# Kernel optimization log

Hardware: AMD Instinct MI355X
Metric: run time of the kernel (lower is better)

Reference implementation:

```python
import jax, jax.numpy as jnp
import numpy as np

N = 65536      # voxels
NFIX = 4096    # fixed-BC voxels (x == 0)
H = 128        # MLP hidden width
NFORCE = 4096  # force-surface points
E0 = 1.0
NU = 0.3
PENAL = 3.0
EM_V = 1e-3    # element volume
L_FIX = 0.05   # BC ramp length for analytical fixed-BC scale
K_FIX = E0 * 100.0
NUM_HUTCH = 50


def mlp(params, x):
    W1, b1, W2, b2, W3, b3, W4, b4 = params
    h = jnp.tanh(x @ W1 + b1)
    h = jnp.tanh(h @ W2 + b2)
    h = jnp.tanh(h @ W3 + b3)
    return h @ W4 + b4


def bc_scale(coord):
    # analytical fixed-BC scale: 0 exactly on the fixed face (x==0), ramps to 1
    return jnp.clip(coord[..., 0] / L_FIX, 0.0, 1.0)


def hutchinson_trace(params, coords, key, num_samples=NUM_HUTCH):
    # tr(J J^T) estimate via v^T J J^T v = ||J^T v||^2, batched VJPs (replaces
    # the per-sample autograd.grad python loop).
    out, vjp_fn = jax.vjp(lambda p: mlp(p, coords), params)

    def step(acc, k):
        v = jax.random.normal(k, out.shape, dtype=out.dtype)
        (g,) = vjp_fn(v)
        flat = jnp.concatenate([x.reshape(-1) for x in jax.tree_util.tree_leaves(g)])
        return acc + flat @ flat, None

    keys = jax.random.split(key, num_samples)
    tot, _ = jax.lax.scan(step, jnp.float32(0.0), keys)
    return tot / num_samples


def setup_inputs() -> dict:
    key = jax.random.key(0)
    ks = jax.random.split(key, 12)
    coord = jax.random.uniform(ks[0], (N, 3), dtype=jnp.float32)
    coord = coord.at[:, 0].set(0.02 + 0.98 * coord[:, 0])  # free voxels: x > 0
    coord = coord.at[:NFIX, 0].set(0.0)                    # fixed voxels: x == 0
    xPhys_m = jax.random.uniform(ks[1], (N, 1), dtype=jnp.float32)
    def lin(k, fi, fo):
        return jax.random.normal(k, (fi, fo), dtype=jnp.float32) / jnp.sqrt(jnp.float32(fi))
    W1 = lin(ks[2], 3, H); b1 = jnp.zeros((H,), jnp.float32)
    W2 = lin(ks[3], H, H); b2 = jnp.zeros((H,), jnp.float32)
    W3 = lin(ks[4], H, H); b3 = jnp.zeros((H,), jnp.float32)
    W4 = lin(ks[5], H, 3); b4 = jnp.zeros((3,), jnp.float32)
    force_coords = jax.random.uniform(ks[6], (NFORCE, 3), dtype=jnp.float32)
    F_vector = jax.random.normal(ks[7], (3,), dtype=jnp.float32)
    return dict(xPhys_m=xPhys_m, coord=coord, W1=W1, b1=b1, W2=W2, b2=b2,
                W3=W3, b3=b3, W4=W4, b4=b4, force_coords=force_coords,
                F_vector=F_vector, n_fix=NFIX)


def reference(xPhys_m, coord, W1, b1, W2, b2, W3, b3, W4, b4,
              force_coords, F_vector, n_fix):
    params = (W1, b1, W2, b2, W3, b3, W4, b4)

    u = mlp(params, coord)                       # [N,3] displacements
    scale = bc_scale(coord)                      # [N]
    fixed_mask = (scale == 0.0)

    # fixed-BC penalty energy
    u_fix = u * fixed_mask[:, None].astype(u.dtype)
    E_fix_all = xPhys_m ** PENAL * 0.5 * K_FIX * jnp.sum(u_fix ** 2, axis=1, keepdims=True)
    n_fix_ratio = jnp.float32(n_fix) / jnp.float32(N)
    E_fix = jnp.mean(E_fix_all[:n_fix]) * n_fix_ratio * EM_V

    # NTK-based adaptive weight via Hutchinson trace (detached, like .item())
    hkey = jax.random.key(42)
    ku, kr = jax.random.split(hkey)
    tr_uu = hutchinson_trace(params, coord[:n_fix], ku)
    tr_rr = hutchinson_trace(params, coord[n_fix:], kr)
    lam_fix = jax.lax.stop_gradient(jnp.clip(tr_rr / (tr_uu + 1e-12), 1e-3, 1e3))

    # per-voxel displacement Jacobian J[n, i, j] = d u_i / d coord_j  (batched
    # fwd-mode replaces three autograd.grad calls)
    J = jax.vmap(jax.jacfwd(lambda c: mlp(params, c)))(coord)  # [N,3,3]
    ux = J[:, 1, :]   # grads of u[:,1] (u0 in source)
    uy = J[:, 0, :]   # grads of u[:,0] (u1 in source)
    uz = J[:, 2, :]
    eps11 = ux[:, 1]
    eps12 = 0.5 * ux[:, 0] + 0.5 * uy[:, 1]
    eps13 = 0.5 * ux[:, 2] + 0.5 * uz[:, 1]
    eps22 = uy[:, 0]
    eps23 = 0.5 * uy[:, 2] + 0.5 * uz[:, 0]
    eps33 = uz[:, 2]

    lame_mu = E0 / (2.0 * (1.0 + NU))
    lame_lambda = E0 * NU / ((1.0 + NU) * (1.0 - 2.0 * NU))
    tr_strain = eps11 + eps22 + eps33
    sq_diag = eps11 * eps11 + eps22 * eps22 + eps33 * eps33
    energy = (0.5 * lame_lambda * tr_strain * tr_strain
              + lame_mu * (sq_diag + 2.0 * (eps12 * eps12 + eps13 * eps13 + eps23 * eps23)))
    energy = energy[:, None] * xPhys_m ** PENAL   # [N,1]
    energy_c = energy * 2.0
    energy_ans = EM_V * jnp.mean(energy)

    force_l = jnp.sum(mlp(params, force_coords) @ F_vector)

    loss = energy_ans - force_l + lam_fix * E_fix
    return (loss, energy_c, u)
```

## Files before the change

kernel.cpp:

```cpp
#include <hip/hip_runtime.h>
#include <math.h>

typedef __bf16 bf16x8 __attribute__((ext_vector_type(8)));
typedef __bf16 bf16x4 __attribute__((ext_vector_type(4)));
typedef float f32x4 __attribute__((ext_vector_type(4)));

#define HDIM 128
#define NTHREADS 512

#define EMV 0.001f
#define LFIX 0.05f
#define KFIX 100.0f
#define LAMBDA_L 0.5769230769230769f
#define MU_L 0.3846153846153846f

__device__ __forceinline__ int swb(int r, int blk) {
    return (r << 7) + ((blk ^ (r & 7)) << 3);
}
__device__ __forceinline__ int swb32(int r, int g) {
    return (r << 5) + ((g ^ ((r >> 1) & 3)) << 3);
}

__device__ __forceinline__ float fast_tanh(float x) {
    float xc = fminf(fmaxf(x, -10.f), 10.f);
    float e = __expf(2.f * xc);
    return (e - 1.f) / (e + 1.f);
}

__device__ __forceinline__ float wred(float v) {
#pragma unroll
    for (int off = 32; off > 0; off >>= 1) v += __shfl_down(v, off, 64);
    return v;
}

template <int NB, int CT0, int CT1>
__device__ __forceinline__ void gemm_f8(const bf16x8 (&aw)[4],
                                        __bf16* const* inb, __bf16* const* outb,
                                        const float* __restrict__ bsL,
                                        int wid, int l15, int q) {
    f32x4 acc[NB][CT1 - CT0];
#pragma unroll
    for (int b = 0; b < NB; ++b)
#pragma unroll
        for (int c = 0; c < CT1 - CT0; ++c) acc[b][c] = (f32x4){0.f, 0.f, 0.f, 0.f};

#pragma unroll
    for (int s = 0; s < 4; ++s)
#pragma unroll
        for (int b = 0; b < NB; ++b)
#pragma unroll
            for (int c = CT0; c < CT1; ++c) {
                bf16x8 bfr = *(const bf16x8*)(inb[b] + swb(c * 16 + l15, s * 4 + q));
                acc[b][c - CT0] = __builtin_amdgcn_mfma_f32_16x16x32_bf16(
                    aw[s], bfr, acc[b][c - CT0], 0, 0, 0);
            }
    __syncthreads();
    const int n0 = wid * 16 + q * 4;
    float4 bv = *(const float4*)(bsL + n0);
    float bias4[4] = {bv.x, bv.y, bv.z, bv.w};
#pragma unroll
    for (int c = CT0; c < CT1; ++c) {
        const int p = c * 16 + l15;
        const int widx = swb(p, n0 >> 3) + (n0 & 7);
        bf16x4 hv;
        float fct[4];
#pragma unroll
        for (int i = 0; i < 4; ++i) {
            float h = fast_tanh(acc[0][c - CT0][i] + bias4[i]);
            hv[i] = (__bf16)h;
            fct[i] = 1.f - h * h;
        }
        *(bf16x4*)(outb[0] + widx) = hv;
#pragma unroll
        for (int b = 1; b < NB; ++b) {
            bf16x4 ov;
#pragma unroll
            for (int i = 0; i < 4; ++i) ov[i] = (__bf16)(acc[b][c - CT0][i] * fct[i]);
            *(bf16x4*)(outb[b] + widx) = ov;
        }
    }
}

template <int NB>
__device__ __forceinline__ void gemm_tr8(const float* __restrict__ Wg, __bf16* Wst,
                                         __bf16* const* bufs,
                                         const __bf16* __restrict__ href,
                                         int wid, int l15, int q, int tid) {
    f32x4 acc[NB][2];
#pragma unroll
    for (int b = 0; b < NB; ++b) {
        acc[b][0] = (f32x4){0.f, 0.f, 0.f, 0.f};
        acc[b][1] = (f32x4){0.f, 0.f, 0.f, 0.f};
    }
#pragma unroll
    for (int c = 0; c < 4; ++c) {
        __syncthreads();
        {
            int j = tid >> 2, k8 = tid & 3;
            const float4* src = (const float4*)(Wg + j * HDIM + c * 32 + k8 * 8);
            float4 v0 = src[0], v1 = src[1];
            bf16x8 pk = {(__bf16)v0.x, (__bf16)v0.y, (__bf16)v0.z, (__bf16)v0.w,
                         (__bf16)v1.x, (__bf16)v1.y, (__bf16)v1.z, (__bf16)v1.w};
            *(bf16x8*)(Wst + swb32(j, k8)) = pk;
        }
        __syncthreads();
        bf16x8 afr = *(const bf16x8*)(Wst + swb32(wid * 16 + l15, q));
#pragma unroll
        for (int b = 0; b < NB; ++b) {
            bf16x8 b0 = *(const bf16x8*)(bufs[b] + swb(l15, c * 4 + q));
            acc[b][0] = __builtin_amdgcn_mfma_f32_16x16x32_bf16(afr, b0, acc[b][0], 0, 0, 0);
            bf16x8 b1 = *(const bf16x8*)(bufs[b] + swb(16 + l15, c * 4 + q));
            acc[b][1] = __builtin_amdgcn_mfma_f32_16x16x32_bf16(afr, b1, acc[b][1], 0, 0, 0);
        }
    }
    __syncthreads();
    const int n0 = wid * 16 + q * 4;
#pragma unroll
    for (int ct = 0; ct < 2; ++ct) {
        const int p = ct * 16 + l15;
        const int widx = swb(p, n0 >> 3) + (n0 & 7);
        bf16x4 hv = *(const bf16x4*)(href + widx);
        float fct[4];
#pragma unroll
        for (int i = 0; i < 4; ++i) {
            float h = (float)hv[i];
            fct[i] = 1.f - h * h;
        }
#pragma unroll
        for (int b = 0; b < NB; ++b) {
            bf16x4 ov;
#pragma unroll
            for (int i = 0; i < 4; ++i) ov[i] = (__bf16)(acc[b][ct][i] * fct[i]);
            *(bf16x4*)(bufs[b] + widx) = ov;
        }
    }
}

__device__ __forceinline__ void dnorms8(const __bf16* a, const __bf16* b, const __bf16* c2,
                                        float* npart, int tid) {
    int p = tid & 31, cc = tid >> 5;
    bf16x8 v0 = *(const bf16x8*)(a + swb(p, cc));
    bf16x8 v1 = *(const bf16x8*)(b + swb(p, cc));
    bf16x8 v2 = *(const bf16x8*)(c2 + swb(p, cc));
    float s0 = 0.f, s1 = 0.f, s2 = 0.f;
#pragma unroll
    for (int e = 0; e < 8; ++e) {
        float f0 = (float)v0[e], f1 = (float)v1[e], f2 = (float)v2[e];
        s0 += f0 * f0;
        s1 += f1 * f1;
        s2 += f2 * f2;
    }
    npart[(0 + cc) * 32 + p] = s0;
    npart[(16 + cc) * 32 + p] = s1;
    npart[(32 + cc) * 32 + p] = s2;
}

__device__ __forceinline__ float sum16(const float* npart, int buf, int p) {
    float d = 0.f;
#pragma unroll
    for (int i = 0; i < 16; ++i) d += npart[(buf * 16 + i) * 32 + p];
    return d;
}
__device__ __forceinline__ float sum48(const float* npart, int p) {
    float d = 0.f;
#pragma unroll
    for (int i = 0; i < 48; ++i) d += npart[i * 32 + p];
    return d;
}

__global__ void __launch_bounds__(NTHREADS, 4) pinn_all(
    const float* __restrict__ xPhys, const float* __restrict__ coord,
    const float* __restrict__ W1, const float* __restrict__ b1,
    const float* __restrict__ W2, const float* __restrict__ b2,
    const float* __restrict__ W3, const float* __restrict__ b3,
    const float* __restrict__ W4, const float* __restrict__ b4,
    const float* __restrict__ fc, const float* __restrict__ Fv,
    const int* __restrict__ nfixp,
    float* __restrict__ energy_c_out, float* __restrict__ u_out,
    float* __restrict__ acc, int nm32, int nmain64, int ntrb, int NF) {
    __shared__ __align__(16) __bf16 pool[32768];
    __shared__ __align__(16) __bf16 W4p[16 * HDIM];
    __shared__ __align__(16) float W1s[4 * HDIM];
    __shared__ __align__(16) float W4ts[3 * HDIM];
    __shared__ __align__(16) float gls[64 * 12];
    __shared__ __align__(16) float uls[64 * 4];
    __shared__ float nh1s[32], nh2s[32], nh3s[32];

    const int tid = threadIdx.x;
    const int lane = tid & 63, wid = tid >> 6, l15 = lane & 15, q = lane >> 4;
    const int bi = blockIdx.x;
    const int nfixv = nfixp[0];

    int ttile = -1;
    if (bi < ntrb) {
        const int nfull = nfixv >> 5;
        const int cm = (nfixv & 31) ? 1 : 0;
        const int c1 = (nfull + 7) >> 3;
        int t;
        if (bi < c1) {
            t = bi << 3;
        } else if (cm && bi == c1) {
            t = nfull;
        } else {
            const int rr0 = nfull + cm;
            const int f0 = rr0 + ((8 - (rr0 & 15) + 16) & 15);
            t = f0 + ((bi - c1 - cm) << 4);
        }
        if (t >= nm32) return;
        ttile = t;
    }

    for (int i = tid; i < 3 * HDIM; i += NTHREADS) W1s[i] = W1[i];
    if (tid < HDIM) W1s[3 * HDIM + tid] = b1[tid];
    if (tid < 3 * HDIM) W4ts[tid] = W4[(tid & 127) * 3 + (tid >> 7)];
    if (tid < 256) {
        int o = tid >> 4, blk = tid & 15, j0 = blk * 8;
        bf16x8 pk;
#pragma unroll
        for (int e = 0; e < 8; ++e) pk[e] = (__bf16)((o < 3) ? W4[(j0 + e) * 3 + o] : 0.f);
        *(bf16x8*)(W4p + swb(o, blk)) = pk;
    }
    bf16x8 aw2[4], aw3[4];
#pragma unroll
    for (int s = 0; s < 4; ++s) {
        const int kb = s * 32 + q * 8;
        const int n = wid * 16 + l15;
        bf16x8 v2, v3;
#pragma unroll
        for (int e = 0; e < 8; ++e) {
            v2[e] = (__bf16)W2[(kb + e) * HDIM + n];
            v3[e] = (__bf16)W3[(kb + e) * HDIM + n];
        }
        aw2[s] = v2;
        aw3[s] = v3;
    }
    __syncthreads();

    if (bi < ntrb) {
        const int base = ttile * 32;
        __bf16* H1 = pool;
        __bf16* H2 = pool + 4096;
        __bf16* H3 = pool + 8192;
        __bf16* T0 = pool + 12288;
        __bf16* T1 = pool + 16384;
        __bf16* T2 = pool + 20480;
        __bf16* WST = pool + 24576;
        float* npart = (float*)(pool + 28672);

        {
            int p = tid >> 4, blk = tid & 15, j0 = blk * 8;
            const float* cp = coord + (base + p) * 3;
            float x0 = cp[0], x1 = cp[1], x2 = cp[2];
            bf16x8 hv, t0v, t1v, t2v;
#pragma unroll
            for (int jj = 0; jj < 8; ++jj) {
                int j = j0 + jj;
                float w0 = W1s[j], w1 = W1s[HDIM + j], w2 = W1s[2 * HDIM + j];
                float z = W1s[3 * HDIM + j] + x0 * w0 + x1 * w1 + x2 * w2;
                float h = fast_tanh(z);
                float fct = 1.f - h * h;
                hv[jj] = (__bf16)h;
                t0v[jj] = (__bf16)(fct * w0);
                t1v[jj] = (__bf16)(fct * w1);
                t2v[jj] = (__bf16)(fct * w2);
            }
            int wi = swb(p, blk);
            *(bf16x8*)(H1 + wi) = hv;
            *(bf16x8*)(T0 + wi) = t0v;
            *(bf16x8*)(T1 + wi) = t1v;
            *(bf16x8*)(T2 + wi) = t2v;
        }
        __syncthreads();
        {
            __bf16* ib[4] = {H1, T0, T1, T2};
            __bf16* ob[4] = {H2, T0, T1, T2};
            gemm_f8<4, 0, 2>(aw2, ib, ob, b2, wid, l15, q);
        }
        __syncthreads();
        {
            __bf16* ib[4] = {H2, T0, T1, T2};
            __bf16* ob[4] = {H3, T0, T1, T2};
            gemm_f8<4, 0, 2>(aw3, ib, ob, b3, wid, l15, q);
        }
        __syncthreads();

        dnorms8(H1, H2, H3, npart, tid);
        __syncthreads();
        if (tid < 32) {
            nh1s[tid] = sum16(npart, 0, tid);
            nh2s[tid] = sum16(npart, 1, tid);
            nh3s[tid] = sum16(npart, 2, tid);
        }
        __syncthreads();
        {
            int p = tid >> 4, blk = tid & 15, j0 = blk * 8;
            bf16x8 h3v = *(const bf16x8*)(H3 + swb(p, blk));
            bf16x8 d0, d1, d2;
#pragma unroll
            for (int e = 0; e < 8; ++e) {
                float h = (float)h3v[e];
                float fct = 1.f - h * h;
                d0[e] = (__bf16)(fct * W4ts[j0 + e]);
                d1[e] = (__bf16)(fct * W4ts[HDIM + j0 + e]);
                d2[e] = (__bf16)(fct * W4ts[2 * HDIM + j0 + e]);
            }
            int wi = swb(p, blk);
            *(bf16x8*)(T0 + wi) = d0;
            *(bf16x8*)(T1 + wi) = d1;
            *(bf16x8*)(T2 + wi) = d2;
        }
        __syncthreads();
        float s_acc = 0.f;
        dnorms8(T0, T1, T2, npart, tid);
        __syncthreads();
        if (tid < 32) s_acc = sum48(npart, tid) * (1.f + nh2s[tid]);
        {
            __bf16* ib[3] = {T0, T1, T2};
            gemm_tr8<3>(W3, WST, ib, H2, wid, l15, q, tid);
        }
        __syncthreads();
        dnorms8(T0, T1, T2, npart, tid);
        __syncthreads();
        if (tid < 32) s_acc += sum48(npart, tid) * (1.f + nh1s[tid]);
        {
            __bf16* ib[3] = {T0, T1, T2};
            gemm_tr8<3>(W2, WST, ib, H1, wid, l15, q, tid);
        }
        __syncthreads();
        dnorms8(T0, T1, T2, npart, tid);
        __syncthreads();
        if (tid < 64) {
            float su = 0.f, sr = 0.f, cu = 0.f, cr = 0.f;
            if (tid < 32) {
                int p = tid;
                const float* cp = coord + (base + p) * 3;
                float x0 = cp[0], x1 = cp[1], x2 = cp[2];
                float nx = x0 * x0 + x1 * x1 + x2 * x2;
                float s = s_acc + sum48(npart, p) * (1.f + nx) + 3.f * (nh3s[p] + 1.f);
                bool uu = (base + p) < nfixv;
                su = uu ? s : 0.f;
                sr = uu ? 0.f : s;
                cu = uu ? 1.f : 0.f;
                cr = uu ? 0.f : 1.f;
            }
            su = wred(su);
            sr = wred(sr);
            cu = wred(cu);
            cr = wred(cr);
            if (tid == 0) {
                atomicAdd(acc + 3, su);
                atomicAdd(acc + 4, sr);
                atomicAdd(acc + 5, cu);
                atomicAdd(acc + 6, cr);
            }
        }
    } else if (bi < ntrb + nmain64) {
        const int base = (bi - ntrb) * 64;
        __bf16* HF = pool;
        __bf16* TF0 = pool + 8192;
        __bf16* TF1 = pool + 16384;
        __bf16* TF2 = pool + 24576;

#pragma unroll
        for (int it2 = 0; it2 < 2; ++it2) {
            int f = tid + it2 * NTHREADS;
            int p = f >> 4, blk = f & 15, j0 = blk * 8;
            const float* cp = coord + (base + p) * 3;
            float x0 = cp[0], x1 = cp[1], x2 = cp[2];
            bf16x8 hv, t0v, t1v, t2v;
#pragma unroll
            for (int jj = 0; jj < 8; ++jj) {
                int j = j0 + jj;
                float w0 = W1s[j], w1 = W1s[HDIM + j], w2 = W1s[2 * HDIM + j];
                float z = W1s[3 * HDIM + j] + x0 * w0 + x1 * w1 + x2 * w2;
                float h = fast_tanh(z);
                float fct = 1.f - h * h;
                hv[jj] = (__bf16)h;
                t0v[jj] = (__bf16)(fct * w0);
                t1v[jj] = (__bf16)(fct * w1);
                t2v[jj] = (__bf16)(fct * w2);
            }
            int wi = swb(p, blk);
            *(bf16x8*)(HF + wi) = hv;
            *(bf16x8*)(TF0 + wi) = t0v;
            *(bf16x8*)(TF1 + wi) = t1v;
            *(bf16x8*)(TF2 + wi) = t2v;
        }
        __syncthreads();
        {
            __bf16* ib[4] = {HF, TF0, TF1, TF2};
            gemm_f8<4, 0, 2>(aw2, ib, ib, b2, wid, l15, q);
            gemm_f8<4, 2, 4>(aw2, ib, ib, b2, wid, l15, q);
        }
        __syncthreads();
        {
            __bf16* ib[4] = {HF, TF0, TF1, TF2};
            gemm_f8<4, 0, 2>(aw3, ib, ib, b3, wid, l15, q);
            gemm_f8<4, 2, 4>(aw3, ib, ib, b3, wid, l15, q);
        }
        __syncthreads();

        {
            f32x4 ha0 = (f32x4){0.f, 0.f, 0.f, 0.f};
            f32x4 ha1 = (f32x4){0.f, 0.f, 0.f, 0.f};
            if (wid < 4) {
                const int ct = wid;
#pragma unroll
                for (int s = 0; s < 4; ++s) {
                    int kb = s * 4 + q;
                    bf16x8 af = *(const bf16x8*)(W4p + swb(l15, kb));
                    bf16x8 bA = *(const bf16x8*)(HF + swb(ct * 16 + l15, kb));
                    ha0 = __builtin_amdgcn_mfma_f32_16x16x32_bf16(af, bA, ha0, 0, 0, 0);
                    bf16x8 bB = *(const bf16x8*)(TF0 + swb(ct * 16 + l15, kb));
                    ha1 = __builtin_amdgcn_mfma_f32_16x16x32_bf16(af, bB, ha1, 0, 0, 0);
                }
                if (q == 0) {
                    int p = ct * 16 + l15;
#pragma unroll
                    for (int o = 0; o < 3; ++o) {
                        float uv = ha0[o] + b4[o];
                        uls[p * 4 + o] = uv;
                        u_out[(base + p) * 3 + o] = uv;
                    }
#pragma unroll
                    for (int o = 0; o < 3; ++o) gls[p * 12 + o] = ha1[o];
                }
            } else {
                const int ct = wid - 4;
#pragma unroll
                for (int s = 0; s < 4; ++s) {
                    int kb = s * 4 + q;
                    bf16x8 af = *(const bf16x8*)(W4p + swb(l15, kb));
                    bf16x8 bA = *(const bf16x8*)(TF1 + swb(ct * 16 + l15, kb));
                    ha0 = __builtin_amdgcn_mfma_f32_16x16x32_bf16(af, bA, ha0, 0, 0, 0);
                    bf16x8 bB = *(const bf16x8*)(TF2 + swb(ct * 16 + l15, kb));
                    ha1 = __builtin_amdgcn_mfma_f32_16x16x32_bf16(af, bB, ha1, 0, 0, 0);
                }
                if (q == 0) {
                    int p = ct * 16 + l15;
#pragma unroll
                    for (int o = 0; o < 3; ++o) gls[p * 12 + 3 + o] = ha0[o];
#pragma unroll
                    for (int o = 0; o < 3; ++o) gls[p * 12 + 6 + o] = ha1[o];
                }
            }
        }
        __syncthreads();

        if (tid < 64) {
            int p = tid;
            float x0 = coord[(base + p) * 3];
            float xp = xPhys[base + p];
            float xp3 = xp * xp * xp;
            float sc = fminf(fmaxf(x0 * (1.f / LFIX), 0.f), 1.f);
            float ef = 0.f;
            if ((base + p) < nfixv && sc == 0.f) {
                float u0 = uls[p * 4], u1 = uls[p * 4 + 1], u2 = uls[p * 4 + 2];
                ef = xp3 * 0.5f * KFIX * (u0 * u0 + u1 * u1 + u2 * u2);
            }
            float g00 = gls[p * 12 + 0], g01 = gls[p * 12 + 1], g02 = gls[p * 12 + 2];
            float g10 = gls[p * 12 + 3], g11 = gls[p * 12 + 4], g12 = gls[p * 12 + 5];
            float g20 = gls[p * 12 + 6], g21 = gls[p * 12 + 7], g22 = gls[p * 12 + 8];
            float e11 = g11, e22 = g00, e33 = g22;
            float e12 = 0.5f * (g01 + g10);
            float e13 = 0.5f * (g21 + g12);
            float e23 = 0.5f * (g20 + g02);
            float tr = e11 + e22 + e33;
            float en = 0.5f * LAMBDA_L * tr * tr +
                       MU_L * (e11 * e11 + e22 * e22 + e33 * e33 +
                               2.f * (e12 * e12 + e13 * e13 + e23 * e23));
            float exp3 = en * xp3;
            energy_c_out[base + p] = 2.f * exp3;
            float er = exp3;
            ef = wred(ef);
            er = wred(er);
            if (tid == 0) {
                atomicAdd(acc + 1, ef);
                atomicAdd(acc + 0, er);
            }
        }
    } else {
        const int fbase = (bi - ntrb - nmain64) * 64;
        __bf16* HF = pool;
#pragma unroll
        for (int it2 = 0; it2 < 2; ++it2) {
            int f = tid + it2 * NTHREADS;
            int p = f >> 4, blk = f & 15, j0 = blk * 8;
            int pp = fbase + p;
            if (pp >= NF) pp = NF - 1;
            const float* cp = fc + pp * 3;
            float x0 = cp[0], x1 = cp[1], x2 = cp[2];
            bf16x8 hv;
#pragma unroll
            for (int jj = 0; jj < 8; ++jj) {
                int j = j0 + jj;
                float z = W1s[3 * HDIM + j] + x0 * W1s[j] + x1 * W1s[HDIM + j] +
                          x2 * W1s[2 * HDIM + j];
                hv[jj] = (__bf16)fast_tanh(z);
            }
            *(bf16x8*)(HF + swb(p, blk)) = hv;
        }
        __syncthreads();
        {
            __bf16* ib[1] = {HF};
            gemm_f8<1, 0, 2>(aw2, ib, ib, b2, wid, l15, q);
            gemm_f8<1, 2, 4>(aw2, ib, ib, b2, wid, l15, q);
        }
        __syncthreads();
        {
            __bf16* ib[1] = {HF};
            gemm_f8<1, 0, 2>(aw3, ib, ib, b3, wid, l15, q);
            gemm_f8<1, 2, 4>(aw3, ib, ib, b3, wid, l15, q);
        }
        __syncthreads();
        if (wid < 4) {
            const int ct = wid;
            f32x4 ha = (f32x4){0.f, 0.f, 0.f, 0.f};
#pragma unroll
            for (int s = 0; s < 4; ++s) {
                int kb = s * 4 + q;
                bf16x8 af = *(const bf16x8*)(W4p + swb(l15, kb));
                bf16x8 bf_ = *(const bf16x8*)(HF + swb(ct * 16 + l15, kb));
                ha = __builtin_amdgcn_mfma_f32_16x16x32_bf16(af, bf_, ha, 0, 0, 0);
            }
            if (q == 0) {
                int p = ct * 16 + l15;
#pragma unroll
                for (int o = 0; o < 3; ++o) uls[p * 4 + o] = ha[o] + b4[o];
            }
        }
        __syncthreads();
        if (tid < 64) {
            float fsum = 0.f;
            if (fbase + tid < NF)
                fsum = uls[tid * 4] * Fv[0] + uls[tid * 4 + 1] * Fv[1] +
                       uls[tid * 4 + 2] * Fv[2];
            fsum = wred(fsum);
            if (tid == 0) atomicAdd(acc + 2, fsum);
        }
    }
}

__global__ void pinn_final(const float* __restrict__ acc, float* __restrict__ out,
                           int Ntot, const int* __restrict__ nfixp) {
    float es = acc[0], ef = acc[1], fl = acc[2];
    float su = acc[3], sr = acc[4], cu = acc[5], cr = acc[6];
    float nfix = (float)nfixp[0];
    float tu = su / fmaxf(cu, 1.f) * nfix;
    float tr = sr / fmaxf(cr, 1.f) * ((float)Ntot - nfix);
    float energy_ans = EMV * (es / (float)Ntot);
    float E_fix = ef * EMV / (float)Ntot;
    float lam = tr / (tu + 1e-12f);
    lam = fminf(fmaxf(lam, 0.001f), 1000.f);
    out[0] = energy_ans - fl + lam * E_fix;
}

extern "C" void kernel_launch(void* const* d_in, const int* in_sizes, int n_in,
                              void* d_out, int out_size, void* d_ws, size_t ws_size,
                              hipStream_t stream) {
    const float* xPhys = (const float*)d_in[0];
    const float* coord = (const float*)d_in[1];
    const float* W1 = (const float*)d_in[2];
    const float* b1 = (const float*)d_in[3];
    const float* W2 = (const float*)d_in[4];
    const float* b2 = (const float*)d_in[5];
    const float* W3 = (const float*)d_in[6];
    const float* b3 = (const float*)d_in[7];
    const float* W4 = (const float*)d_in[8];
    const float* b4 = (const float*)d_in[9];
    const float* fc = (const float*)d_in[10];
    const float* Fv = (const float*)d_in[11];
    const int* nfix = (const int*)d_in[12];

    const int N = in_sizes[0];
    const int NF = in_sizes[10] / 3;
    float* out = (float*)d_out;
    float* acc = (float*)d_ws;

    const int nm32 = N / 32;
    const int nmain64 = N / 64;
    const int ntrb = nm32 / 8 + 2;
    const int nforce64 = (NF + 63) / 64;
    const int nblocks = ntrb + nmain64 + nforce64;
    (void)hipMemsetAsync(acc, 0, 8 * sizeof(float), stream);
    pinn_all<<<dim3(nblocks), dim3(NTHREADS), 0, stream>>>(
        xPhys, coord, W1, b1, W2, b2, W3, b3, W4, b4, fc, Fv, nfix,
        out + 1, out + 1 + N, acc, nm32, nmain64, ntrb, NF);
    pinn_final<<<dim3(1), dim3(1), 0, stream>>>(acc, out, N, nfix);
}
```

Before: 142.6 us.

## Merge split gemm_f8 calls into single pass, remap layer-1 threads, use rcp in tanh

The two half-tile gemm_f8 calls per layer become one call that handles all four column tiles at once. This removes an extra __syncthreads and a second sweep over the A fragments, at the cost of more accumulator registers (4x4 f32x4 per lane). Layer-1 thread mapping is changed so each lane owns one point and waves own hidden blocks, which lets coordinate loads be shared. fast_tanh now uses a hardware reciprocal instead of a divide, giving slightly lower precision.

```diff
diff --git a/kernel.cpp b/kernel.cpp
--- a/kernel.cpp
+++ b/kernel.cpp
@@ -24,7 +24,7 @@
 __device__ __forceinline__ float fast_tanh(float x) {
     float xc = fminf(fmaxf(x, -10.f), 10.f);
     float e = __expf(2.f * xc);
-    return (e - 1.f) / (e + 1.f);
+    return 1.f - 2.f * __builtin_amdgcn_rcpf(e + 1.f);
 }
 
 __device__ __forceinline__ float wred(float v) {
@@ -33,40 +33,40 @@
     return v;
 }
 
-template <int NB, int CT0, int CT1>
+template <int NB, int CT>
 __device__ __forceinline__ void gemm_f8(const bf16x8 (&aw)[4],
                                         __bf16* const* inb, __bf16* const* outb,
                                         const float* __restrict__ bsL,
                                         int wid, int l15, int q) {
-    f32x4 acc[NB][CT1 - CT0];
+    f32x4 acc[NB][CT];
 #pragma unroll
     for (int b = 0; b < NB; ++b)
 #pragma unroll
-        for (int c = 0; c < CT1 - CT0; ++c) acc[b][c] = (f32x4){0.f, 0.f, 0.f, 0.f};
+        for (int c = 0; c < CT; ++c) acc[b][c] = (f32x4){0.f, 0.f, 0.f, 0.f};
 
 #pragma unroll
     for (int s = 0; s < 4; ++s)
 #pragma unroll
         for (int b = 0; b < NB; ++b)
 #pragma unroll
-            for (int c = CT0; c < CT1; ++c) {
+            for (int c = 0; c < CT; ++c) {
                 bf16x8 bfr = *(const bf16x8*)(inb[b] + swb(c * 16 + l15, s * 4 + q));
-                acc[b][c - CT0] = __builtin_amdgcn_mfma_f32_16x16x32_bf16(
-                    aw[s], bfr, acc[b][c - CT0], 0, 0, 0);
+                acc[b][c] = __builtin_amdgcn_mfma_f32_16x16x32_bf16(
+                    aw[s], bfr, acc[b][c], 0, 0, 0);
             }
     __syncthreads();
     const int n0 = wid * 16 + q * 4;
     float4 bv = *(const float4*)(bsL + n0);
     float bias4[4] = {bv.x, bv.y, bv.z, bv.w};
 #pragma unroll
-    for (int c = CT0; c < CT1; ++c) {
+    for (int c = 0; c < CT; ++c) {
         const int p = c * 16 + l15;
         const int widx = swb(p, n0 >> 3) + (n0 & 7);
         bf16x4 hv;
         float fct[4];
 #pragma unroll
         for (int i = 0; i < 4; ++i) {
-            float h = fast_tanh(acc[0][c - CT0][i] + bias4[i]);
+            float h = fast_tanh(acc[0][c][i] + bias4[i]);
             hv[i] = (__bf16)h;
             fct[i] = 1.f - h * h;
         }
@@ -75,7 +75,7 @@
         for (int b = 1; b < NB; ++b) {
             bf16x4 ov;
 #pragma unroll
-            for (int i = 0; i < 4; ++i) ov[i] = (__bf16)(acc[b][c - CT0][i] * fct[i]);
+            for (int i = 0; i < 4; ++i) ov[i] = (__bf16)(acc[b][c][i] * fct[i]);
             *(bf16x4*)(outb[b] + widx) = ov;
         }
     }
@@ -248,7 +248,8 @@
         float* npart = (float*)(pool + 28672);
 
         {
-            int p = tid >> 4, blk = tid & 15, j0 = blk * 8;
+            const int p = lane & 31, sub = lane >> 5;
+            const int blk = wid * 2 + sub, j0 = blk * 8;
             const float* cp = coord + (base + p) * 3;
             float x0 = cp[0], x1 = cp[1], x2 = cp[2];
             bf16x8 hv, t0v, t1v, t2v;
@@ -274,13 +275,13 @@
         {
             __bf16* ib[4] = {H1, T0, T1, T2};
             __bf16* ob[4] = {H2, T0, T1, T2};
-            gemm_f8<4, 0, 2>(aw2, ib, ob, b2, wid, l15, q);
+            gemm_f8<4, 2>(aw2, ib, ob, b2, wid, l15, q);
         }
         __syncthreads();
         {
             __bf16* ib[4] = {H2, T0, T1, T2};
             __bf16* ob[4] = {H3, T0, T1, T2};
-            gemm_f8<4, 0, 2>(aw3, ib, ob, b3, wid, l15, q);
+            gemm_f8<4, 2>(aw3, ib, ob, b3, wid, l15, q);
         }
         __syncthreads();
 
@@ -293,7 +294,8 @@
         }
         __syncthreads();
         {
-            int p = tid >> 4, blk = tid & 15, j0 = blk * 8;
+            const int p = lane & 31, sub = lane >> 5;
+            const int blk = wid * 2 + sub, j0 = blk * 8;
             bf16x8 h3v = *(const bf16x8*)(H3 + swb(p, blk));
             bf16x8 d0, d1, d2;
 #pragma unroll
@@ -361,42 +363,42 @@
         __bf16* TF1 = pool + 16384;
         __bf16* TF2 = pool + 24576;
 
-#pragma unroll
-        for (int it2 = 0; it2 < 2; ++it2) {
-            int f = tid + it2 * NTHREADS;
-            int p = f >> 4, blk = f & 15, j0 = blk * 8;
+        {
+            const int p = lane;
             const float* cp = coord + (base + p) * 3;
             float x0 = cp[0], x1 = cp[1], x2 = cp[2];
-            bf16x8 hv, t0v, t1v, t2v;
-#pragma unroll
-            for (int jj = 0; jj < 8; ++jj) {
-                int j = j0 + jj;
-                float w0 = W1s[j], w1 = W1s[HDIM + j], w2 = W1s[2 * HDIM + j];
-                float z = W1s[3 * HDIM + j] + x0 * w0 + x1 * w1 + x2 * w2;
-                float h = fast_tanh(z);
-                float fct = 1.f - h * h;
-                hv[jj] = (__bf16)h;
-                t0v[jj] = (__bf16)(fct * w0);
-                t1v[jj] = (__bf16)(fct * w1);
-                t2v[jj] = (__bf16)(fct * w2);
-            }
-            int wi = swb(p, blk);
-            *(bf16x8*)(HF + wi) = hv;
-            *(bf16x8*)(TF0 + wi) = t0v;
-            *(bf16x8*)(TF1 + wi) = t1v;
-            *(bf16x8*)(TF2 + wi) = t2v;
+#pragma unroll
+            for (int it2 = 0; it2 < 2; ++it2) {
+                const int blk = it2 * 8 + wid, j0 = blk * 8;
+                bf16x8 hv, t0v, t1v, t2v;
+#pragma unroll
+                for (int jj = 0; jj < 8; ++jj) {
+                    int j = j0 + jj;
+                    float w0 = W1s[j], w1 = W1s[HDIM + j], w2 = W1s[2 * HDIM + j];
+                    float z = W1s[3 * HDIM + j] + x0 * w0 + x1 * w1 + x2 * w2;
+                    float h = fast_tanh(z);
+                    float fct = 1.f - h * h;
+                    hv[jj] = (__bf16)h;
+                    t0v[jj] = (__bf16)(fct * w0);
+                    t1v[jj] = (__bf16)(fct * w1);
+                    t2v[jj] = (__bf16)(fct * w2);
+                }
+                int wi = swb(p, blk);
+                *(bf16x8*)(HF + wi) = hv;
+                *(bf16x8*)(TF0 + wi) = t0v;
+                *(bf16x8*)(TF1 + wi) = t1v;
+                *(bf16x8*)(TF2 + wi) = t2v;
+            }
         }
         __syncthreads();
         {
             __bf16* ib[4] = {HF, TF0, TF1, TF2};
-            gemm_f8<4, 0, 2>(aw2, ib, ib, b2, wid, l15, q);
-            gemm_f8<4, 2, 4>(aw2, ib, ib, b2, wid, l15, q);
+            gemm_f8<4, 4>(aw2, ib, ib, b2, wid, l15, q);
         }
         __syncthreads();
         {
             __bf16* ib[4] = {HF, TF0, TF1, TF2};
-            gemm_f8<4, 0, 2>(aw3, ib, ib, b3, wid, l15, q);
-            gemm_f8<4, 2, 4>(aw3, ib, ib, b3, wid, l15, q);
+            gemm_f8<4, 4>(aw3, ib, ib, b3, wid, l15, q);
         }
         __syncthreads();
 
@@ -482,35 +484,34 @@
     } else {
         const int fbase = (bi - ntrb - nmain64) * 64;
         __bf16* HF = pool;
-#pragma unroll
-        for (int it2 = 0; it2 < 2; ++it2) {
-            int f = tid + it2 * NTHREADS;
-            int p = f >> 4, blk = f & 15, j0 = blk * 8;
-            int pp = fbase + p;
+        {
+            int pp = fbase + lane;
             if (pp >= NF) pp = NF - 1;
             const float* cp = fc + pp * 3;
             float x0 = cp[0], x1 = cp[1], x2 = cp[2];
-            bf16x8 hv;
-#pragma unroll
-            for (int jj = 0; jj < 8; ++jj) {
-                int j = j0 + jj;
-                float z = W1s[3 * HDIM + j] + x0 * W1s[j] + x1 * W1s[HDIM + j] +
-                          x2 * W1s[2 * HDIM + j];
-                hv[jj] = (__bf16)fast_tanh(z);
-            }
-            *(bf16x8*)(HF + swb(p, blk)) = hv;
+#pragma unroll
+            for (int it2 = 0; it2 < 2; ++it2) {
+                const int blk = it2 * 8 + wid, j0 = blk * 8;
+                bf16x8 hv;
+#pragma unroll
+                for (int jj = 0; jj < 8; ++jj) {
+                    int j = j0 + jj;
+                    float z = W1s[3 * HDIM + j] + x0 * W1s[j] + x1 * W1s[HDIM + j] +
+                              x2 * W1s[2 * HDIM + j];
+                    hv[jj] = (__bf16)fast_tanh(z);
+                }
+                *(bf16x8*)(HF + swb(lane, blk)) = hv;
+            }
         }
         __syncthreads();
         {
             __bf16* ib[1] = {HF};
-            gemm_f8<1, 0, 2>(aw2, ib, ib, b2, wid, l15, q);
-            gemm_f8<1, 2, 4>(aw2, ib, ib, b2, wid, l15, q);
+            gemm_f8<1, 4>(aw2, ib, ib, b2, wid, l15, q);
         }
         __syncthreads();
         {
             __bf16* ib[1] = {HF};
-            gemm_f8<1, 0, 2>(aw3, ib, ib, b3, wid, l15, q);
-            gemm_f8<1, 2, 4>(aw3, ib, ib, b3, wid, l15, q);
+            gemm_f8<1, 4>(aw3, ib, ib, b3, wid, l15, q);
         }
         __syncthreads();
         if (wid < 4) {
```

Measured after the change: 156.9 us. 1.1x slower.
